# Performance work log

Measured on AMD Instinct MI355X. Metric: run time of the kernel, lower is better.

Reference implementation:

```python
import jax, jax.numpy as jnp
import numpy as np

B, S, E, H = 4, 1024, 1024, 16
HD = E // H  # head_dim = 64


def setup_inputs() -> dict:
    key = jax.random.key(0)
    ks = jax.random.split(key, 7)
    return {
        "query": jax.random.normal(ks[0], (B, S, E), dtype=jnp.float32),
        "key": jax.random.normal(ks[1], (B, S, E), dtype=jnp.float32),
        "value": jax.random.normal(ks[2], (B, S, E), dtype=jnp.float32),
        # per-head Linear weights stacked: [H, head_dim, emb_dim] (torch Linear is y = x @ W^T)
        "Wq": jax.random.normal(ks[3], (H, HD, E), dtype=jnp.float32) * (E ** -0.5),
        "Wk": jax.random.normal(ks[4], (H, HD, E), dtype=jnp.float32) * (E ** -0.5),
        "Wv": jax.random.normal(ks[5], (H, HD, E), dtype=jnp.float32) * (E ** -0.5),
        "Wo": jax.random.normal(ks[6], (E, E), dtype=jnp.float32) * (E ** -0.5),
    }


def reference(query, key, value, Wq, Wk, Wv, Wo):
    # Project per head (all heads vectorized): [B,S,E] x [H,HD,E] -> [B,H,S,HD]
    Q = jnp.einsum('bse,hde->bhsd', query, Wq)
    K = jnp.einsum('bse,hde->bhsd', key, Wk)
    V = jnp.einsum('bse,hde->bhsd', value, Wv)
    scale = 1.0 / np.sqrt(HD)  # source divides by sqrt(emb_dim / n_head)
    scores = jnp.einsum('bhsd,bhtd->bhst', Q, K) * scale  # [B,H,S,S]
    p = jax.nn.softmax(scores, axis=-1)
    ctx = jnp.einsum('bhst,bhtd->bhsd', p, V)  # [B,H,S,HD]
    # concat heads along feature dim -> [B,S,E]
    concat = ctx.transpose(0, 2, 1, 3).reshape(query.shape[0], query.shape[1], -1)
    return concat @ Wo.T
```

## Files before the change

### kernel.cpp

```cpp
#include <hip/hip_runtime.h>

typedef __bf16 bf16_t;
typedef __bf16 bf16x4 __attribute__((ext_vector_type(4)));
typedef __bf16 bf16x8 __attribute__((ext_vector_type(8)));
typedef float f32x4 __attribute__((ext_vector_type(4)));
typedef short short4v __attribute__((ext_vector_type(4)));

#define E_DIM 1024
#define S_LEN 1024
#define NHEAD 16
#define HD_DIM 64
#define BATCH 4
#define TOKENS 4096

__device__ __forceinline__ void async_copy16(const bf16_t* g, bf16_t* l) {
    __builtin_amdgcn_global_load_lds((const __attribute__((address_space(1))) void*)g,
                                     (__attribute__((address_space(3))) void*)l,
                                     16, 0, 0);
}

__device__ __forceinline__ f32x4 pv_mfma(bf16x4 a, bf16x4 b, f32x4 c) {
#if __has_builtin(__builtin_amdgcn_mfma_f32_16x16x16_bf16)
    return __builtin_amdgcn_mfma_f32_16x16x16_bf16(a, b, c, 0, 0, 0);
#elif __has_builtin(__builtin_amdgcn_mfma_f32_16x16x16bf16_1k)
    short4v as, bs;
    __builtin_memcpy(&as, &a, 8);
    __builtin_memcpy(&bs, &b, 8);
    return __builtin_amdgcn_mfma_f32_16x16x16bf16_1k(as, bs, c, 0, 0, 0);
#else
    f32x4 d;
    asm volatile("v_mfma_f32_16x16x16_bf16 %0, %1, %2, %3\n\ts_nop 7\n\ts_nop 7"
                 : "=v"(d)
                 : "v"(a), "v"(b), "v"(c));
    return d;
#endif
}

__device__ __forceinline__ void stage_tiles(const bf16_t* gA, const bf16_t* gB,
                                            bf16_t* sAbuf, bf16_t* sBbuf,
                                            int wave, int k0) {
    const int K = 1024;
#pragma unroll
    for (int cc = 0; cc < 4; cc++) {
        int c = wave * 4 + cc;
        if (c < 8)
            async_copy16(gA + (size_t)c * 16 * K + k0, sAbuf + c * 16 * 32);
        else
            async_copy16(gB + (size_t)(c - 8) * 16 * K + k0, sBbuf + (c - 8) * 16 * 32);
    }
}

__global__ __launch_bounds__(256) void cast_all(const float* __restrict__ q,
                                                const float* __restrict__ k,
                                                const float* __restrict__ v,
                                                const float* __restrict__ wq,
                                                const float* __restrict__ wk,
                                                const float* __restrict__ wv,
                                                const float* __restrict__ wo,
                                                bf16_t* __restrict__ dst) {
    const size_t NX = (size_t)TOKENS * E_DIM;
    const size_t NW = (size_t)E_DIM * E_DIM;
    size_t i = ((size_t)blockIdx.x * 256 + threadIdx.x) * 8;
    const float* src;
    size_t off;
    if (i < 3 * NX) {
        int a = (int)(i >> 22);
        src = a == 0 ? q : (a == 1 ? k : v);
        off = i & (NX - 1);
    } else {
        size_t j = i - 3 * NX;
        int a = (int)(j >> 20);
        src = a == 0 ? wq : (a == 1 ? wk : (a == 2 ? wv : wo));
        off = j & (NW - 1);
    }
    float4 x = *(const float4*)(src + off);
    float4 y = *(const float4*)(src + off + 4);
    bf16x8 o;
    o[0] = (bf16_t)x.x; o[1] = (bf16_t)x.y; o[2] = (bf16_t)x.z; o[3] = (bf16_t)x.w;
    o[4] = (bf16_t)y.x; o[5] = (bf16_t)y.y; o[6] = (bf16_t)y.z; o[7] = (bf16_t)y.w;
    *(bf16x8*)(dst + i) = o;
}

__global__ __launch_bounds__(256, 4) void proj_gemm(const bf16_t* __restrict__ Xq,
                                                    const bf16_t* __restrict__ Xk,
                                                    const bf16_t* __restrict__ Xv,
                                                    const bf16_t* __restrict__ Wq,
                                                    const bf16_t* __restrict__ Wk,
                                                    const bf16_t* __restrict__ Wv,
                                                    bf16_t* __restrict__ Qp,
                                                    bf16_t* __restrict__ Kp,
                                                    bf16_t* __restrict__ Vp) {
    __shared__ bf16_t sA[2][128 * 32];
    __shared__ bf16_t sB[2][128 * 32];
    const int z = blockIdx.z;
    const bf16_t* A = z == 0 ? Xq : (z == 1 ? Xk : Xv);
    const bf16_t* B = z == 0 ? Wq : (z == 1 ? Wk : Wv);
    bf16_t* C = z == 0 ? Qp : (z == 1 ? Kp : Vp);
    const int N = 1024, K = 1024;
    const int lid = blockIdx.x + 8 * blockIdx.y;
    const int m0 = (((lid & 7) << 2) + ((lid >> 3) & 3)) * 128;
    const int n0 = (lid >> 5) * 128;

    const int tid = threadIdx.x;
    const int wave = tid >> 6, lane = tid & 63;
    const int quad = lane >> 4, l16 = lane & 15;
    const int wm = (wave >> 1) * 64, wn = (wave & 1) * 64;
    const int srow = lane >> 2, scol = (lane & 3) * 8;

    const bf16_t* gA = A + (size_t)(m0 + srow) * K + scol;
    const bf16_t* gB = B + (size_t)(n0 + srow) * K + scol;

    f32x4 acc[4][4];
    const f32x4 vzero = {0.f, 0.f, 0.f, 0.f};
#pragma unroll
    for (int mt = 0; mt < 4; mt++)
#pragma unroll
        for (int nt = 0; nt < 4; nt++) acc[mt][nt] = vzero;

    stage_tiles(gA, gB, sA[0], sB[0], wave, 0);
    asm volatile("s_waitcnt vmcnt(0)" ::: "memory");
    __syncthreads();

    int cur = 0;
    for (int k0 = 32; k0 < K; k0 += 32) {
        stage_tiles(gA, gB, sA[cur ^ 1], sB[cur ^ 1], wave, k0);

        bf16x8 af[4], bfr[4];
#pragma unroll
        for (int mt = 0; mt < 4; mt++)
            af[mt] = *(const bf16x8*)&sA[cur][(wm + mt * 16 + l16) * 32 + quad * 8];
#pragma unroll
        for (int nt = 0; nt < 4; nt++)
            bfr[nt] = *(const bf16x8*)&sB[cur][(wn + nt * 16 + l16) * 32 + quad * 8];
#pragma unroll
        for (int mt = 0; mt < 4; mt++)
#pragma unroll
            for (int nt = 0; nt < 4; nt++)
                acc[mt][nt] = __builtin_amdgcn_mfma_f32_16x16x32_bf16(af[mt], bfr[nt],
                                                                      acc[mt][nt], 0, 0, 0);

        asm volatile("s_waitcnt vmcnt(0)" ::: "memory");
        __syncthreads();
        cur ^= 1;
    }

    {
        bf16x8 af[4], bfr[4];
#pragma unroll
        for (int mt = 0; mt < 4; mt++)
            af[mt] = *(const bf16x8*)&sA[cur][(wm + mt * 16 + l16) * 32 + quad * 8];
#pragma unroll
        for (int nt = 0; nt < 4; nt++)
            bfr[nt] = *(const bf16x8*)&sB[cur][(wn + nt * 16 + l16) * 32 + quad * 8];
#pragma unroll
        for (int mt = 0; mt < 4; mt++)
#pragma unroll
            for (int nt = 0; nt < 4; nt++)
                acc[mt][nt] = __builtin_amdgcn_mfma_f32_16x16x32_bf16(af[mt], bfr[nt],
                                                                      acc[mt][nt], 0, 0, 0);
    }

#pragma unroll
    for (int mt = 0; mt < 4; mt++)
#pragma unroll
        for (int nt = 0; nt < 4; nt++)
#pragma unroll
            for (int r = 0; r < 4; r++) {
                int row = m0 + wm + mt * 16 + quad * 4 + r;
                int col = n0 + wn + nt * 16 + l16;
                C[(size_t)row * N + col] = (bf16_t)acc[mt][nt][r];
            }
}

__global__ __launch_bounds__(256, 4) void out_gemm(const bf16_t* __restrict__ A,
                                                   const bf16_t* __restrict__ B,
                                                   float* __restrict__ C) {
    __shared__ bf16_t sA[2][128 * 32];
    __shared__ bf16_t sB[2][64 * 32];
    const int N = 1024, K = 1024;
    const int wgid = blockIdx.x * 64 + blockIdx.y;
    const int m0 = (wgid >> 4) * 128;
    const int n0 = (wgid & 15) * 64;

    const int tid = threadIdx.x;
    const int wave = tid >> 6, lane = tid & 63;
    const int quad = lane >> 4, l16 = lane & 15;
    const int wm = (wave >> 1) * 64, wn = (wave & 1) * 32;
    const int srow = lane >> 2, scol = (lane & 3) * 8;

    const bf16_t* gA = A + (size_t)(m0 + srow) * K + scol;
    const bf16_t* gB = B + (size_t)(n0 + srow) * K + scol;

    f32x4 acc[4][2];
    const f32x4 vzero = {0.f, 0.f, 0.f, 0.f};
#pragma unroll
    for (int mt = 0; mt < 4; mt++)
#pragma unroll
        for (int nt = 0; nt < 2; nt++) acc[mt][nt] = vzero;

#define OUT_STAGE(sa, sb, k0)                                                  \
    {                                                                          \
        _Pragma("unroll") for (int cc = 0; cc < 3; cc++) {                     \
            int c = wave * 3 + cc;                                             \
            if (c < 8)                                                         \
                async_copy16(gA + (size_t)c * 16 * K + (k0), (sa) + c * 16 * 32); \
            else                                                               \
                async_copy16(gB + (size_t)(c - 8) * 16 * K + (k0),             \
                             (sb) + (c - 8) * 16 * 32);                        \
        }                                                                      \
    }

    OUT_STAGE(sA[0], sB[0], 0);
    asm volatile("s_waitcnt vmcnt(0)" ::: "memory");
    __syncthreads();

    int cur = 0;
    for (int k0 = 32; k0 < K; k0 += 32) {
        OUT_STAGE(sA[cur ^ 1], sB[cur ^ 1], k0);

        bf16x8 af[4], bfr[2];
#pragma unroll
        for (int mt = 0; mt < 4; mt++)
            af[mt] = *(const bf16x8*)&sA[cur][(wm + mt * 16 + l16) * 32 + quad * 8];
#pragma unroll
        for (int nt = 0; nt < 2; nt++)
            bfr[nt] = *(const bf16x8*)&sB[cur][(wn + nt * 16 + l16) * 32 + quad * 8];
#pragma unroll
        for (int mt = 0; mt < 4; mt++)
#pragma unroll
            for (int nt = 0; nt < 2; nt++)
                acc[mt][nt] = __builtin_amdgcn_mfma_f32_16x16x32_bf16(af[mt], bfr[nt],
                                                                      acc[mt][nt], 0, 0, 0);

        asm volatile("s_waitcnt vmcnt(0)" ::: "memory");
        __syncthreads();
        cur ^= 1;
    }

    {
        bf16x8 af[4], bfr[2];
#pragma unroll
        for (int mt = 0; mt < 4; mt++)
            af[mt] = *(const bf16x8*)&sA[cur][(wm + mt * 16 + l16) * 32 + quad * 8];
#pragma unroll
        for (int nt = 0; nt < 2; nt++)
            bfr[nt] = *(const bf16x8*)&sB[cur][(wn + nt * 16 + l16) * 32 + quad * 8];
#pragma unroll
        for (int mt = 0; mt < 4; mt++)
#pragma unroll
            for (int nt = 0; nt < 2; nt++)
                acc[mt][nt] = __builtin_amdgcn_mfma_f32_16x16x32_bf16(af[mt], bfr[nt],
                                                                      acc[mt][nt], 0, 0, 0);
    }

#pragma unroll
    for (int mt = 0; mt < 4; mt++)
#pragma unroll
        for (int nt = 0; nt < 2; nt++)
#pragma unroll
            for (int r = 0; r < 4; r++) {
                int row = m0 + wm + mt * 16 + quad * 4 + r;
                int col = n0 + wn + nt * 16 + l16;
                C[(size_t)row * N + col] = acc[mt][nt][r];
            }
#undef OUT_STAGE
}

#define KP 72

__global__ __launch_bounds__(256, 4) void flash_attn(const bf16_t* __restrict__ Q,
                                                     const bf16_t* __restrict__ K,
                                                     const bf16_t* __restrict__ V,
                                                     bf16_t* __restrict__ O) {
    __shared__ bf16_t smem[2][2 * 64 * KP];

    const int tid = threadIdx.x;
    const int wave = tid >> 6, lane = tid & 63;
    const int quad = lane >> 4, l16 = lane & 15;
    const int qt = blockIdx.y >> 1;
    const int h = blockIdx.x * 2 + (blockIdx.y & 1);
    const int b = blockIdx.z;
    const size_t base = (size_t)b * S_LEN * E_DIM + h * HD_DIM;
    const float c_exp = 0.125f * 1.44269504089f;

    const int qrow = qt * 64 + wave * 16 + l16;
    bf16x8 qf[2];
    {
        const bf16_t* qp = Q + base + (size_t)qrow * E_DIM + quad * 8;
        qf[0] = *(const bf16x8*)qp;
        qf[1] = *(const bf16x8*)(qp + 32);
    }

    float lsum = 0.f;
    f32x4 acc[4];
    const f32x4 vzero = {0.f, 0.f, 0.f, 0.f};
#pragma unroll
    for (int dt = 0; dt < 4; dt++) acc[dt] = vzero;

    const int stg = tid & 7;
    const int r0 = tid >> 3;
    const int c0 = stg * 8;
    const bf16_t* Kbase = K + base + (size_t)r0 * E_DIM + c0;
    const bf16_t* Vbase = V + base + (size_t)r0 * E_DIM + c0;

    bf16x8 kvn[2], vvn[2];
#pragma unroll
    for (int it = 0; it < 2; it++) {
        kvn[it] = *(const bf16x8*)(Kbase + (size_t)it * 32 * E_DIM);
        vvn[it] = *(const bf16x8*)(Vbase + (size_t)it * 32 * E_DIM);
    }
    {
        bf16_t* dK = smem[0];
        bf16_t* dVt = smem[0] + 64 * KP;
#pragma unroll
        for (int it = 0; it < 2; it++) {
            int r = r0 + it * 32;
            *(bf16x8*)&dK[r * KP + c0] = kvn[it];
            int jb = (((r >> 2) ^ stg) << 2) | (r & 3);
#pragma unroll
            for (int i = 0; i < 8; i++) dVt[(c0 + i) * KP + jb] = vvn[it][i];
        }
    }

    int cur = 0;
    for (int j0 = 0; j0 < S_LEN; j0 += 64) {
        const bool more = (j0 + 64 < S_LEN);
        if (more) {
#pragma unroll
            for (int it = 0; it < 2; it++) {
                kvn[it] = *(const bf16x8*)(Kbase + (size_t)(j0 + 64 + it * 32) * E_DIM);
                vvn[it] = *(const bf16x8*)(Vbase + (size_t)(j0 + 64 + it * 32) * E_DIM);
            }
        }
        __syncthreads();
        const bf16_t* sK = smem[cur];
        const bf16_t* sVt = smem[cur] + 64 * KP;

        bf16x8 kf[4][2];
#pragma unroll
        for (int jt = 0; jt < 4; jt++) {
            kf[jt][0] = *(const bf16x8*)&sK[(jt * 16 + l16) * KP + quad * 8];
            kf[jt][1] = *(const bf16x8*)&sK[(jt * 16 + l16) * KP + 32 + quad * 8];
        }

        bf16x4 pb[4];
#pragma unroll
        for (int jt = 0; jt < 4; jt++) {
            f32x4 s = vzero;
            s = __builtin_amdgcn_mfma_f32_16x16x32_bf16(kf[jt][0], qf[0], s, 0, 0, 0);
            s = __builtin_amdgcn_mfma_f32_16x16x32_bf16(kf[jt][1], qf[1], s, 0, 0, 0);
#pragma unroll
            for (int r = 0; r < 4; r++) {
                float p = __builtin_amdgcn_exp2f(s[r] * c_exp);
                lsum += p;
                pb[jt][r] = (bf16_t)p;
            }
        }

#pragma unroll
        for (int jt = 0; jt < 4; jt++)
#pragma unroll
            for (int dt = 0; dt < 4; dt++) {
                int cidx = (jt * 4 + quad) ^ (dt * 2 + (l16 >> 3));
                bf16x4 vf = *(const bf16x4*)&sVt[(dt * 16 + l16) * KP + cidx * 4];
                acc[dt] = pv_mfma(vf, pb[jt], acc[dt]);
            }

        if (more) {
            bf16_t* dK = smem[cur ^ 1];
            bf16_t* dVt = smem[cur ^ 1] + 64 * KP;
#pragma unroll
            for (int it = 0; it < 2; it++) {
                int r = r0 + it * 32;
                *(bf16x8*)&dK[r * KP + c0] = kvn[it];
                int jb = (((r >> 2) ^ stg) << 2) | (r & 3);
#pragma unroll
                for (int i = 0; i < 8; i++) dVt[(c0 + i) * KP + jb] = vvn[it][i];
            }
        }
        cur ^= 1;
    }

    lsum += __shfl_xor(lsum, 16);
    lsum += __shfl_xor(lsum, 32);
    const float inv = __builtin_amdgcn_rcpf(lsum);

    __syncthreads();
    bf16_t* ep = smem[0] + wave * 16 * KP;
#pragma unroll
    for (int dt = 0; dt < 4; dt++)
#pragma unroll
        for (int r = 0; r < 4; r++)
            ep[l16 * KP + dt * 16 + quad * 4 + r] = (bf16_t)(acc[dt][r] * inv);
#pragma unroll
    for (int c = 0; c < 2; c++) {
        int row = lane >> 2;
        int col = (lane & 3) * 8 + c * 32;
        bf16x8 oval = *(const bf16x8*)&ep[row * KP + col];
        *(bf16x8*)&O[base + (size_t)(qt * 64 + wave * 16 + row) * E_DIM + col] = oval;
    }
}

extern "C" void kernel_launch(void* const* d_in, const int* in_sizes, int n_in,
                              void* d_out, int out_size, void* d_ws, size_t ws_size,
                              hipStream_t stream) {
    const float* q  = (const float*)d_in[0];
    const float* k  = (const float*)d_in[1];
    const float* v  = (const float*)d_in[2];
    const float* wq = (const float*)d_in[3];
    const float* wk = (const float*)d_in[4];
    const float* wv = (const float*)d_in[5];
    const float* wo = (const float*)d_in[6];
    float* out = (float*)d_out;

    const int NX = TOKENS * E_DIM;
    const int NW = E_DIM * E_DIM;

    bf16_t* ws  = (bf16_t*)d_ws;
    bf16_t* Xq  = ws;
    bf16_t* Xk  = ws + (size_t)NX;
    bf16_t* Xv  = ws + (size_t)2 * NX;
    bf16_t* Wqb = ws + (size_t)3 * NX;
    bf16_t* Wkb = Wqb + NW;
    bf16_t* Wvb = Wkb + NW;
    bf16_t* Wob = Wvb + NW;
    bf16_t* Qp  = Wob + NW;
    bf16_t* Kp  = Qp + (size_t)NX;
    bf16_t* Vp  = Kp + (size_t)NX;
    bf16_t* ctx = Xq;

    cast_all<<<8192, 256, 0, stream>>>(q, k, v, wq, wk, wv, wo, Xq);

    proj_gemm<<<dim3(8, 32, 3), 256, 0, stream>>>(Xq, Xk, Xv, Wqb, Wkb, Wvb, Qp, Kp, Vp);

    flash_attn<<<dim3(8, 32, 4), 256, 0, stream>>>(Qp, Kp, Vp, ctx);

    out_gemm<<<dim3(8, 64), 256, 0, stream>>>(ctx, Wob, out);
}
```

Baseline: 198.2 us.

## Fuse activation fp32-to-bf16 cast into projection GEMM and enlarge out_gemm tiles

```diff
diff --git a/kernel.cpp b/kernel.cpp
--- a/kernel.cpp
+++ b/kernel.cpp
@@ -13,7 +13,7 @@
 #define BATCH 4
 #define TOKENS 4096
 
-__device__ __forceinline__ void async_copy16(const bf16_t* g, bf16_t* l) {
+__device__ __forceinline__ void async_copy16(const void* g, void* l) {
     __builtin_amdgcn_global_load_lds((const __attribute__((address_space(1))) void*)g,
                                      (__attribute__((address_space(3))) void*)l,
                                      16, 0, 0);
@@ -50,29 +50,16 @@
     }
 }
 
-__global__ __launch_bounds__(256) void cast_all(const float* __restrict__ q,
-                                                const float* __restrict__ k,
-                                                const float* __restrict__ v,
-                                                const float* __restrict__ wq,
-                                                const float* __restrict__ wk,
-                                                const float* __restrict__ wv,
-                                                const float* __restrict__ wo,
-                                                bf16_t* __restrict__ dst) {
-    const size_t NX = (size_t)TOKENS * E_DIM;
+__global__ __launch_bounds__(256) void cast_w(const float* __restrict__ wq,
+                                              const float* __restrict__ wk,
+                                              const float* __restrict__ wv,
+                                              const float* __restrict__ wo,
+                                              bf16_t* __restrict__ dst) {
     const size_t NW = (size_t)E_DIM * E_DIM;
     size_t i = ((size_t)blockIdx.x * 256 + threadIdx.x) * 8;
-    const float* src;
-    size_t off;
-    if (i < 3 * NX) {
-        int a = (int)(i >> 22);
-        src = a == 0 ? q : (a == 1 ? k : v);
-        off = i & (NX - 1);
-    } else {
-        size_t j = i - 3 * NX;
-        int a = (int)(j >> 20);
-        src = a == 0 ? wq : (a == 1 ? wk : (a == 2 ? wv : wo));
-        off = j & (NW - 1);
-    }
+    int a = (int)(i >> 20);
+    const float* src = a == 0 ? wq : (a == 1 ? wk : (a == 2 ? wv : wo));
+    size_t off = i & (NW - 1);
     float4 x = *(const float4*)(src + off);
     float4 y = *(const float4*)(src + off + 4);
     bf16x8 o;
@@ -81,19 +68,19 @@
     *(bf16x8*)(dst + i) = o;
 }
 
-__global__ __launch_bounds__(256, 4) void proj_gemm(const bf16_t* __restrict__ Xq,
-                                                    const bf16_t* __restrict__ Xk,
-                                                    const bf16_t* __restrict__ Xv,
+__global__ __launch_bounds__(256, 3) void proj_gemm(const float* __restrict__ Xq,
+                                                    const float* __restrict__ Xk,
+                                                    const float* __restrict__ Xv,
                                                     const bf16_t* __restrict__ Wq,
                                                     const bf16_t* __restrict__ Wk,
                                                     const bf16_t* __restrict__ Wv,
                                                     bf16_t* __restrict__ Qp,
                                                     bf16_t* __restrict__ Kp,
                                                     bf16_t* __restrict__ Vp) {
-    __shared__ bf16_t sA[2][128 * 32];
+    __shared__ float sAf[2][128 * 32];
     __shared__ bf16_t sB[2][128 * 32];
     const int z = blockIdx.z;
-    const bf16_t* A = z == 0 ? Xq : (z == 1 ? Xk : Xv);
+    const float* A = z == 0 ? Xq : (z == 1 ? Xk : Xv);
     const bf16_t* B = z == 0 ? Wq : (z == 1 ? Wk : Wv);
     bf16_t* C = z == 0 ? Qp : (z == 1 ? Kp : Vp);
     const int N = 1024, K = 1024;
@@ -105,10 +92,10 @@
     const int wave = tid >> 6, lane = tid & 63;
     const int quad = lane >> 4, l16 = lane & 15;
     const int wm = (wave >> 1) * 64, wn = (wave & 1) * 64;
-    const int srow = lane >> 2, scol = (lane & 3) * 8;
-
-    const bf16_t* gA = A + (size_t)(m0 + srow) * K + scol;
-    const bf16_t* gB = B + (size_t)(n0 + srow) * K + scol;
+
+    const int arow = lane >> 3;
+    const int acol = ((lane & 7) ^ ((arow & 3) << 1)) * 4;
+    const int brow = lane >> 2, bcol = (lane & 3) * 8;
 
     f32x4 acc[4][4];
     const f32x4 vzero = {0.f, 0.f, 0.f, 0.f};
@@ -117,48 +104,57 @@
 #pragma unroll
         for (int nt = 0; nt < 4; nt++) acc[mt][nt] = vzero;
 
-    stage_tiles(gA, gB, sA[0], sB[0], wave, 0);
+#define PROJ_STAGE(buf, k0)                                                          \
+    {                                                                                \
+        _Pragma("unroll") for (int cc = 0; cc < 6; cc++) {                           \
+            int c = wave * 6 + cc;                                                   \
+            if (c < 16)                                                              \
+                async_copy16(A + (size_t)(m0 + c * 8 + arow) * K + (k0) + acol,      \
+                             &sAf[buf][c * 256]);                                    \
+            else {                                                                   \
+                int cb = c - 16;                                                     \
+                async_copy16(B + (size_t)(n0 + cb * 16 + brow) * K + (k0) + bcol,    \
+                             &sB[buf][cb * 512]);                                    \
+            }                                                                        \
+        }                                                                            \
+    }
+
+    PROJ_STAGE(0, 0);
     asm volatile("s_waitcnt vmcnt(0)" ::: "memory");
     __syncthreads();
 
+#define PROJ_COMPUTE(cur)                                                            \
+    {                                                                                \
+        bf16x8 af[4], bfr[4];                                                        \
+        _Pragma("unroll") for (int mt = 0; mt < 4; mt++) {                           \
+            int r = wm + mt * 16 + l16;                                              \
+            const float* pa = &sAf[cur][r * 32 + ((quad ^ (l16 & 3)) * 8)];          \
+            f32x4 a0 = *(const f32x4*)pa;                                            \
+            f32x4 a1 = *(const f32x4*)(pa + 4);                                      \
+            bf16x8 t;                                                                \
+            _Pragma("unroll") for (int i = 0; i < 4; i++) {                          \
+                t[i] = (bf16_t)a0[i];                                                \
+                t[4 + i] = (bf16_t)a1[i];                                            \
+            }                                                                        \
+            af[mt] = t;                                                              \
+        }                                                                            \
+        _Pragma("unroll") for (int nt = 0; nt < 4; nt++)                             \
+            bfr[nt] = *(const bf16x8*)&sB[cur][(wn + nt * 16 + l16) * 32 + quad * 8];\
+        _Pragma("unroll") for (int mt = 0; mt < 4; mt++)                             \
+            _Pragma("unroll") for (int nt = 0; nt < 4; nt++)                         \
+                acc[mt][nt] = __builtin_amdgcn_mfma_f32_16x16x32_bf16(               \
+                    af[mt], bfr[nt], acc[mt][nt], 0, 0, 0);                          \
+    }
+
     int cur = 0;
     for (int k0 = 32; k0 < K; k0 += 32) {
-        stage_tiles(gA, gB, sA[cur ^ 1], sB[cur ^ 1], wave, k0);
-
-        bf16x8 af[4], bfr[4];
-#pragma unroll
-        for (int mt = 0; mt < 4; mt++)
-            af[mt] = *(const bf16x8*)&sA[cur][(wm + mt * 16 + l16) * 32 + quad * 8];
-#pragma unroll
-        for (int nt = 0; nt < 4; nt++)
-            bfr[nt] = *(const bf16x8*)&sB[cur][(wn + nt * 16 + l16) * 32 + quad * 8];
-#pragma unroll
-        for (int mt = 0; mt < 4; mt++)
-#pragma unroll
-            for (int nt = 0; nt < 4; nt++)
-                acc[mt][nt] = __builtin_amdgcn_mfma_f32_16x16x32_bf16(af[mt], bfr[nt],
-                                                                      acc[mt][nt], 0, 0, 0);
-
+        PROJ_STAGE(cur ^ 1, k0);
+        PROJ_COMPUTE(cur);
         asm volatile("s_waitcnt vmcnt(0)" ::: "memory");
         __syncthreads();
         cur ^= 1;
     }
-
-    {
-        bf16x8 af[4], bfr[4];
-#pragma unroll
-        for (int mt = 0; mt < 4; mt++)
-            af[mt] = *(const bf16x8*)&sA[cur][(wm + mt * 16 + l16) * 32 + quad * 8];
-#pragma unroll
-        for (int nt = 0; nt < 4; nt++)
-            bfr[nt] = *(const bf16x8*)&sB[cur][(wn + nt * 16 + l16) * 32 + quad * 8];
-#pragma unroll
-        for (int mt = 0; mt < 4; mt++)
-#pragma unroll
-            for (int nt = 0; nt < 4; nt++)
-                acc[mt][nt] = __builtin_amdgcn_mfma_f32_16x16x32_bf16(af[mt], bfr[nt],
-                                                                      acc[mt][nt], 0, 0, 0);
-    }
+    PROJ_COMPUTE(cur);
 
 #pragma unroll
     for (int mt = 0; mt < 4; mt++)
@@ -170,65 +166,55 @@
                 int col = n0 + wn + nt * 16 + l16;
                 C[(size_t)row * N + col] = (bf16_t)acc[mt][nt][r];
             }
+#undef PROJ_STAGE
+#undef PROJ_COMPUTE
 }
 
 __global__ __launch_bounds__(256, 4) void out_gemm(const bf16_t* __restrict__ A,
                                                    const bf16_t* __restrict__ B,
                                                    float* __restrict__ C) {
     __shared__ bf16_t sA[2][128 * 32];
-    __shared__ bf16_t sB[2][64 * 32];
+    __shared__ bf16_t sB[2][128 * 32];
     const int N = 1024, K = 1024;
-    const int wgid = blockIdx.x * 64 + blockIdx.y;
-    const int m0 = (wgid >> 4) * 128;
-    const int n0 = (wgid & 15) * 64;
+    const int lid = blockIdx.x + 8 * blockIdx.y;
+    const int m0 = (((lid & 7) << 2) + ((lid >> 3) & 3)) * 128;
+    const int n0 = (lid >> 5) * 128;
 
     const int tid = threadIdx.x;
     const int wave = tid >> 6, lane = tid & 63;
     const int quad = lane >> 4, l16 = lane & 15;
-    const int wm = (wave >> 1) * 64, wn = (wave & 1) * 32;
+    const int wm = (wave >> 1) * 64, wn = (wave & 1) * 64;
     const int srow = lane >> 2, scol = (lane & 3) * 8;
 
     const bf16_t* gA = A + (size_t)(m0 + srow) * K + scol;
     const bf16_t* gB = B + (size_t)(n0 + srow) * K + scol;
 
-    f32x4 acc[4][2];
+    f32x4 acc[4][4];
     const f32x4 vzero = {0.f, 0.f, 0.f, 0.f};
 #pragma unroll
     for (int mt = 0; mt < 4; mt++)
 #pragma unroll
-        for (int nt = 0; nt < 2; nt++) acc[mt][nt] = vzero;
-
-#define OUT_STAGE(sa, sb, k0)                                                  \
-    {                                                                          \
-        _Pragma("unroll") for (int cc = 0; cc < 3; cc++) {                     \
-            int c = wave * 3 + cc;                                             \
-            if (c < 8)                                                         \
-                async_copy16(gA + (size_t)c * 16 * K + (k0), (sa) + c * 16 * 32); \
-            else                                                               \
-                async_copy16(gB + (size_t)(c - 8) * 16 * K + (k0),             \
-                             (sb) + (c - 8) * 16 * 32);                        \
-        }                                                                      \
-    }
-
-    OUT_STAGE(sA[0], sB[0], 0);
+        for (int nt = 0; nt < 4; nt++) acc[mt][nt] = vzero;
+
+    stage_tiles(gA, gB, sA[0], sB[0], wave, 0);
     asm volatile("s_waitcnt vmcnt(0)" ::: "memory");
     __syncthreads();
 
     int cur = 0;
     for (int k0 = 32; k0 < K; k0 += 32) {
-        OUT_STAGE(sA[cur ^ 1], sB[cur ^ 1], k0);
-
-        bf16x8 af[4], bfr[2];
+        stage_tiles(gA, gB, sA[cur ^ 1], sB[cur ^ 1], wave, k0);
+
+        bf16x8 af[4], bfr[4];
 #pragma unroll
         for (int mt = 0; mt < 4; mt++)
             af[mt] = *(const bf16x8*)&sA[cur][(wm + mt * 16 + l16) * 32 + quad * 8];
 #pragma unroll
-        for (int nt = 0; nt < 2; nt++)
+        for (int nt = 0; nt < 4; nt++)
             bfr[nt] = *(const bf16x8*)&sB[cur][(wn + nt * 16 + l16) * 32 + quad * 8];
 #pragma unroll
         for (int mt = 0; mt < 4; mt++)
 #pragma unroll
-            for (int nt = 0; nt < 2; nt++)
+            for (int nt = 0; nt < 4; nt++)
                 acc[mt][nt] = __builtin_amdgcn_mfma_f32_16x16x32_bf16(af[mt], bfr[nt],
                                                                       acc[mt][nt], 0, 0, 0);
 
@@ -238,17 +224,17 @@
     }
 
     {
-        bf16x8 af[4], bfr[2];
+        bf16x8 af[4], bfr[4];
 #pragma unroll
         for (int mt = 0; mt < 4; mt++)
             af[mt] = *(const bf16x8*)&sA[cur][(wm + mt * 16 + l16) * 32 + quad * 8];
 #pragma unroll
-        for (int nt = 0; nt < 2; nt++)
+        for (int nt = 0; nt < 4; nt++)
             bfr[nt] = *(const bf16x8*)&sB[cur][(wn + nt * 16 + l16) * 32 + quad * 8];
 #pragma unroll
         for (int mt = 0; mt < 4; mt++)
 #pragma unroll
-            for (int nt = 0; nt < 2; nt++)
+            for (int nt = 0; nt < 4; nt++)
                 acc[mt][nt] = __builtin_amdgcn_mfma_f32_16x16x32_bf16(af[mt], bfr[nt],
                                                                       acc[mt][nt], 0, 0, 0);
     }
@@ -256,14 +242,13 @@
 #pragma unroll
     for (int mt = 0; mt < 4; mt++)
 #pragma unroll
-        for (int nt = 0; nt < 2; nt++)
+        for (int nt = 0; nt < 4; nt++)
 #pragma unroll
             for (int r = 0; r < 4; r++) {
                 int row = m0 + wm + mt * 16 + quad * 4 + r;
                 int col = n0 + wn + nt * 16 + l16;
                 C[(size_t)row * N + col] = acc[mt][nt][r];
             }
-#undef OUT_STAGE
 }
 
 #define KP 72
@@ -417,23 +402,20 @@
     const int NW = E_DIM * E_DIM;
 
     bf16_t* ws  = (bf16_t*)d_ws;
-    bf16_t* Xq  = ws;
-    bf16_t* Xk  = ws + (size_t)NX;
-    bf16_t* Xv  = ws + (size_t)2 * NX;
-    bf16_t* Wqb = ws + (size_t)3 * NX;
+    bf16_t* Wqb = ws;
     bf16_t* Wkb = Wqb + NW;
     bf16_t* Wvb = Wkb + NW;
     bf16_t* Wob = Wvb + NW;
     bf16_t* Qp  = Wob + NW;
     bf16_t* Kp  = Qp + (size_t)NX;
     bf16_t* Vp  = Kp + (size_t)NX;
-    bf16_t* ctx = Xq;
-
-    cast_all<<<8192, 256, 0, stream>>>(q, k, v, wq, wk, wv, wo, Xq);
-
-    proj_gemm<<<dim3(8, 32, 3), 256, 0, stream>>>(Xq, Xk, Xv, Wqb, Wkb, Wvb, Qp, Kp, Vp);
+    bf16_t* ctx = Vp + (size_t)NX;
+
+    cast_w<<<2048, 256, 0, stream>>>(wq, wk, wv, wo, Wqb);
+
+    proj_gemm<<<dim3(8, 32, 3), 256, 0, stream>>>(q, k, v, Wqb, Wkb, Wvb, Qp, Kp, Vp);
 
     flash_attn<<<dim3(8, 32, 4), 256, 0, stream>>>(Qp, Kp, Vp, ctx);
 
-    out_gemm<<<dim3(8, 64), 256, 0, stream>>>(ctx, Wob, out);
-}
+    out_gemm<<<dim3(8, 32), 256, 0, stream>>>(ctx, Wob, out);
+}
```

Measured after the change: 205.8 us. +3.8%, slower.
